# Kernel optimization log

Measured on AMD Instinct MI355X. Metric: run time of the kernel, lower is better.

Reference implementation:

```python
import jax, jax.numpy as jnp
from jax import lax
import numpy as np

B, T, H, FUT = 2048, 1024, 128, 64

def setup_inputs() -> dict:
    key = jax.random.key(0)
    ks = jax.random.split(key, 7)
    s = 1.0 / np.sqrt(H)
    return {
        "x": jax.random.normal(ks[0], (B, T), dtype=jnp.float32),
        "W_ih": jax.random.uniform(ks[1], (H, 1), jnp.float32, -s, s),
        "W_hh": jax.random.uniform(ks[2], (H, H), jnp.float32, -s, s),
        "b_ih": jax.random.uniform(ks[3], (H,), jnp.float32, -s, s),
        "b_hh": jax.random.uniform(ks[4], (H,), jnp.float32, -s, s),
        "W_out": jax.random.uniform(ks[5], (1, H), jnp.float32, -s, s),
        "b_out": jax.random.uniform(ks[6], (1,), jnp.float32, -s, s),
        "future": FUT,
    }

def reference(x, W_ih, W_hh, b_ih, b_hh, W_out, b_out, future):
    n_samples = x.shape[0]
    n_hidden = W_hh.shape[0]
    h0 = jnp.zeros((n_samples, n_hidden), dtype=x.dtype)
    bias = b_ih + b_hh  # [H]

    def cell(h, inp):  # inp: [B] scalar input per sample
        # RNNCell: h' = tanh(x @ W_ih^T + b_ih + h @ W_hh^T + b_hh)
        h_new = jnp.tanh(inp[:, None] * W_ih[:, 0][None, :] + h @ W_hh.T + bias)
        out = h_new @ W_out.T + b_out  # [B, 1]
        return h_new, out[:, 0]

    # Teacher-forced steps over the input sequence
    h_last, outs = lax.scan(cell, h0, x.T)  # outs: [T, B]

    def fstep(carry, _):
        h, o = carry
        h_new, o_new = cell(h, o)
        return (h_new, o_new), o_new

    (_, _), fouts = lax.scan(fstep, (h_last, outs[-1]), None, length=future)  # [future, B]

    return jnp.concatenate([outs, fouts], axis=0).T  # [B, T+future]
```

## Files before the change

### kernel.cpp

```cpp
#include <hip/hip_runtime.h>
#include <stdint.h>
#include <math.h>


#define TLEN  1024
#define FUT   64
#define HID   128
#define SPB   4
#define NT    256
#define NSTEP (TLEN + FUT)

typedef float f32x4 __attribute__((ext_vector_type(4)));
typedef _Float16 f16x8 __attribute__((ext_vector_type(8)));
typedef uint32_t u32x4 __attribute__((ext_vector_type(4)));

__device__ __forceinline__ f16x8 asf16(u32x4 v) {
    return __builtin_bit_cast(f16x8, v);
}
__device__ __forceinline__ float fast_tanh(float v) {
    return 1.0f - 2.0f / (__expf(2.0f * v) + 1.0f);
}

__global__ __launch_bounds__(NT, 2) void rnn_kernel(
    const float* __restrict__ x,
    const float* __restrict__ W_ih,
    const float* __restrict__ W_hh,
    const float* __restrict__ b_ih,
    const float* __restrict__ b_hh,
    const float* __restrict__ W_out,
    const float* __restrict__ b_out,
    float* __restrict__ out)
{
    __shared__ __align__(16) unsigned short hbuf[2][SPB * HID];
    __shared__ __align__(16) float xstg[128][8];
    __shared__ __align__(16) float ring[2][SPB][68];

    const int tid  = threadIdx.x;
    const int lane = tid & 63;
    const int wid  = tid >> 6;
    const int l15  = lane & 15;
    const int g    = lane >> 4;
    const int s0   = blockIdx.x * SPB;

    const int j0 = 32 * wid + l15;
    const int j1 = j0 + 16;
    f16x8 W0[4], W1[4], Wo[4];
    {
        const float* r0 = W_hh + (size_t)j0 * HID;
        const float* r1 = W_hh + (size_t)j1 * HID;
        #pragma unroll
        for (int kt = 0; kt < 4; ++kt) {
            #pragma unroll
            for (int e = 0; e < 8; ++e) {
                const int k = 16 * e + 4 * kt + g;
                W0[kt][e] = (_Float16)r0[k];
                W1[kt][e] = (_Float16)r1[k];
                Wo[kt][e] = (l15 == 0) ? (_Float16)W_out[k] : (_Float16)0.0f;
            }
        }
    }
    const float bias0 = b_ih[j0] + b_hh[j0];
    const float bias1 = b_ih[j1] + b_hh[j1];
    const float wih0  = W_ih[j0], wih1 = W_ih[j1];
    const float bo    = b_out[0];

    const int s_ = l15 >> 2;
    int aoff[4];
    #pragma unroll
    for (int kt = 0; kt < 4; ++kt)
        aoff[kt] = s_ * 256 + (((4 * kt + g) * 16) ^ (s_ << 5));
    const int woff = g * 256 + ((l15 * 16 + wid * 4) ^ (g << 5));

    for (int idx = tid; idx < SPB * HID; idx += NT)
        ((uint32_t*)hbuf)[idx] = 0;
    __syncthreads();

    u32x4 A_[4];
    #pragma unroll
    for (int kt = 0; kt < 4; ++kt) A_[kt] = (u32x4){0, 0, 0, 0};

    #pragma unroll 2
    for (int i = 0; i < TLEN; ++i) {
        const int p = i & 1;

        if ((i & 127) == 0) {
            #pragma unroll
            for (int pass = 0; pass < 2; ++pass) {
                const int idx = pass * NT + tid;
                const int t = idx & 127, s = idx >> 7;
                xstg[t][s] = x[(size_t)(s0 + s) * TLEN + (i + t)];
            }
            __syncthreads();
        }
        if (i > 64 && (i & 63) == 1 && tid < 16 * SPB) {
            const int q = ((i - 65) >> 6) & 1;
            const int s = tid >> 4, c4 = (tid & 15) * 4;
            const f32x4 v = *(const f32x4*)&ring[q][s][c4];
            *(f32x4*)&out[(size_t)(s0 + s) * NSTEP + (i - 65) + c4] = v;
        }

        const char* hb = (const char*)hbuf[p];
        if ((l15 & 3) == 0) {
            #pragma unroll
            for (int kt = 0; kt < 4; ++kt)
                A_[kt] = *(const u32x4*)(hb + aoff[kt]);
        }

        f32x4 sA = {0.f,0.f,0.f,0.f}, sB = sA;
        #pragma unroll
        for (int kt = 0; kt < 4; ++kt) {
            sA = __builtin_amdgcn_mfma_f32_16x16x32_f16(asf16(A_[kt]), W0[kt], sA, 0, 0, 0);
            sB = __builtin_amdgcn_mfma_f32_16x16x32_f16(asf16(A_[kt]), W1[kt], sB, 0, 0, 0);
        }
        if (wid == 0) {
            f32x4 ov = {0.f,0.f,0.f,0.f};
            #pragma unroll
            for (int kt = 0; kt < 4; ++kt)
                ov = __builtin_amdgcn_mfma_f32_16x16x32_f16(asf16(A_[kt]), Wo[kt], ov, 0, 0, 0);
            if (i > 0 && l15 == 0)
                ring[((i - 1) >> 6) & 1][g][(i - 1) & 63] = ov[0] + bo;
        }

        const float in = xstg[i & 127][g];
        const float h0 = fast_tanh(sA[0] + bias0 + in * wih0);
        const float h1 = fast_tanh(sB[0] + bias1 + in * wih1);
        const uint32_t pv = (uint32_t)__builtin_bit_cast(unsigned short, (_Float16)h0)
                          | ((uint32_t)__builtin_bit_cast(unsigned short, (_Float16)h1) << 16);
        *(uint32_t*)((char*)hbuf[p ^ 1] + woff) = pv;

        __syncthreads();
    }

    #pragma unroll 2
    for (int i = TLEN; i < NSTEP; ++i) {
        const int p = i & 1;

        if ((i & 63) == 1 && tid < 16 * SPB) {
            const int q = ((i - 65) >> 6) & 1;
            const int s = tid >> 4, c4 = (tid & 15) * 4;
            const f32x4 v = *(const f32x4*)&ring[q][s][c4];
            *(f32x4*)&out[(size_t)(s0 + s) * NSTEP + (i - 65) + c4] = v;
        }

        const char* hb = (const char*)hbuf[p];
        if ((l15 & 3) == 0) {
            #pragma unroll
            for (int kt = 0; kt < 4; ++kt)
                A_[kt] = *(const u32x4*)(hb + aoff[kt]);
        }

        f32x4 sA = {0.f,0.f,0.f,0.f}, sB = sA, ov = sA;
        #pragma unroll
        for (int kt = 0; kt < 4; ++kt) {
            sA = __builtin_amdgcn_mfma_f32_16x16x32_f16(asf16(A_[kt]), W0[kt], sA, 0, 0, 0);
            sB = __builtin_amdgcn_mfma_f32_16x16x32_f16(asf16(A_[kt]), W1[kt], sB, 0, 0, 0);
            ov = __builtin_amdgcn_mfma_f32_16x16x32_f16(asf16(A_[kt]), Wo[kt], ov, 0, 0, 0);
        }
        const float oval = ov[0] + bo;
        if (wid == 0 && l15 == 0)
            ring[((i - 1) >> 6) & 1][g][(i - 1) & 63] = oval;

        const float in = __shfl(oval, g << 4);
        const float h0 = fast_tanh(sA[0] + bias0 + in * wih0);
        const float h1 = fast_tanh(sB[0] + bias1 + in * wih1);
        const uint32_t pv = (uint32_t)__builtin_bit_cast(unsigned short, (_Float16)h0)
                          | ((uint32_t)__builtin_bit_cast(unsigned short, (_Float16)h1) << 16);
        *(uint32_t*)((char*)hbuf[p ^ 1] + woff) = pv;

        __syncthreads();
    }

    {
        const char* hb = (const char*)hbuf[NSTEP & 1];
        if ((l15 & 3) == 0) {
            #pragma unroll
            for (int kt = 0; kt < 4; ++kt)
                A_[kt] = *(const u32x4*)(hb + aoff[kt]);
        }
        f32x4 ov = {0.f,0.f,0.f,0.f};
        #pragma unroll
        for (int kt = 0; kt < 4; ++kt)
            ov = __builtin_amdgcn_mfma_f32_16x16x32_f16(asf16(A_[kt]), Wo[kt], ov, 0, 0, 0);
        if (wid == 0 && l15 == 0)
            ring[0][g][63] = ov[0] + bo;
    }
    __syncthreads();
    if (tid < 16 * SPB) {
        const int s = tid >> 4, c4 = (tid & 15) * 4;
        const f32x4 v = *(const f32x4*)&ring[0][s][c4];
        *(f32x4*)&out[(size_t)(s0 + s) * NSTEP + TLEN + c4] = v;
    }
}

extern "C" void kernel_launch(void* const* d_in, const int* in_sizes, int n_in,
                              void* d_out, int out_size, void* d_ws, size_t ws_size,
                              hipStream_t stream) {
    const float* x     = (const float*)d_in[0];
    const float* W_ih  = (const float*)d_in[1];
    const float* W_hh  = (const float*)d_in[2];
    const float* b_ih  = (const float*)d_in[3];
    const float* b_hh  = (const float*)d_in[4];
    const float* W_out = (const float*)d_in[5];
    const float* b_out = (const float*)d_in[6];
    float* out = (float*)d_out;

    dim3 grid(2048 / SPB);
    dim3 block(NT);
    rnn_kernel<<<grid, block, 0, stream>>>(x, W_ih, W_hh, b_ih, b_hh,
                                           W_out, b_out, out);
}
```

Baseline: 391.2 us.

## Split hidden units across 8 waves with one MFMA tile per wave

```diff
diff --git a/kernel.cpp b/kernel.cpp
--- a/kernel.cpp
+++ b/kernel.cpp
@@ -7,7 +7,7 @@
 #define FUT   64
 #define HID   128
 #define SPB   4
-#define NT    256
+#define NT    512
 #define NSTEP (TLEN + FUT)
 
 typedef float f32x4 __attribute__((ext_vector_type(4)));
@@ -21,7 +21,7 @@
     return 1.0f - 2.0f / (__expf(2.0f * v) + 1.0f);
 }
 
-__global__ __launch_bounds__(NT, 2) void rnn_kernel(
+__global__ __launch_bounds__(NT, 4) void rnn_kernel(
     const float* __restrict__ x,
     const float* __restrict__ W_ih,
     const float* __restrict__ W_hh,
@@ -42,26 +42,22 @@
     const int g    = lane >> 4;
     const int s0   = blockIdx.x * SPB;
 
-    const int j0 = 32 * wid + l15;
-    const int j1 = j0 + 16;
-    f16x8 W0[4], W1[4], Wo[4];
+    const int j = 16 * wid + l15;
+    f16x8 W0[4], Wo[4];
     {
-        const float* r0 = W_hh + (size_t)j0 * HID;
-        const float* r1 = W_hh + (size_t)j1 * HID;
+        const float* r0 = W_hh + (size_t)j * HID;
         #pragma unroll
         for (int kt = 0; kt < 4; ++kt) {
             #pragma unroll
             for (int e = 0; e < 8; ++e) {
                 const int k = 16 * e + 4 * kt + g;
                 W0[kt][e] = (_Float16)r0[k];
-                W1[kt][e] = (_Float16)r1[k];
                 Wo[kt][e] = (l15 == 0) ? (_Float16)W_out[k] : (_Float16)0.0f;
             }
         }
     }
-    const float bias0 = b_ih[j0] + b_hh[j0];
-    const float bias1 = b_ih[j1] + b_hh[j1];
-    const float wih0  = W_ih[j0], wih1 = W_ih[j1];
+    const float bias0 = b_ih[j] + b_hh[j];
+    const float wih0  = W_ih[j];
     const float bo    = b_out[0];
 
     const int s_ = l15 >> 2;
@@ -69,7 +65,7 @@
     #pragma unroll
     for (int kt = 0; kt < 4; ++kt)
         aoff[kt] = s_ * 256 + (((4 * kt + g) * 16) ^ (s_ << 5));
-    const int woff = g * 256 + ((l15 * 16 + wid * 4) ^ (g << 5));
+    const int woff = g * 256 + ((l15 * 16 + 2 * wid) ^ (g << 5));
 
     for (int idx = tid; idx < SPB * HID; idx += NT)
         ((uint32_t*)hbuf)[idx] = 0;
@@ -84,12 +80,8 @@
         const int p = i & 1;
 
         if ((i & 127) == 0) {
-            #pragma unroll
-            for (int pass = 0; pass < 2; ++pass) {
-                const int idx = pass * NT + tid;
-                const int t = idx & 127, s = idx >> 7;
-                xstg[t][s] = x[(size_t)(s0 + s) * TLEN + (i + t)];
-            }
+            const int t = tid & 127, s = tid >> 7;
+            xstg[t][s] = x[(size_t)(s0 + s) * TLEN + (i + t)];
             __syncthreads();
         }
         if (i > 64 && (i & 63) == 1 && tid < 16 * SPB) {
@@ -106,27 +98,20 @@
                 A_[kt] = *(const u32x4*)(hb + aoff[kt]);
         }
 
-        f32x4 sA = {0.f,0.f,0.f,0.f}, sB = sA;
+        f32x4 sA = {0.f,0.f,0.f,0.f}, ov = sA;
         #pragma unroll
         for (int kt = 0; kt < 4; ++kt) {
             sA = __builtin_amdgcn_mfma_f32_16x16x32_f16(asf16(A_[kt]), W0[kt], sA, 0, 0, 0);
-            sB = __builtin_amdgcn_mfma_f32_16x16x32_f16(asf16(A_[kt]), W1[kt], sB, 0, 0, 0);
+            ov = __builtin_amdgcn_mfma_f32_16x16x32_f16(asf16(A_[kt]), Wo[kt], ov, 0, 0, 0);
         }
-        if (wid == 0) {
-            f32x4 ov = {0.f,0.f,0.f,0.f};
-            #pragma unroll
-            for (int kt = 0; kt < 4; ++kt)
-                ov = __builtin_amdgcn_mfma_f32_16x16x32_f16(asf16(A_[kt]), Wo[kt], ov, 0, 0, 0);
-            if (i > 0 && l15 == 0)
-                ring[((i - 1) >> 6) & 1][g][(i - 1) & 63] = ov[0] + bo;
-        }
+
+        if (i > 0 && wid == 0 && l15 == 0)
+            ring[((i - 1) >> 6) & 1][g][(i - 1) & 63] = ov[0] + bo;
 
         const float in = xstg[i & 127][g];
         const float h0 = fast_tanh(sA[0] + bias0 + in * wih0);
-        const float h1 = fast_tanh(sB[0] + bias1 + in * wih1);
-        const uint32_t pv = (uint32_t)__builtin_bit_cast(unsigned short, (_Float16)h0)
-                          | ((uint32_t)__builtin_bit_cast(unsigned short, (_Float16)h1) << 16);
-        *(uint32_t*)((char*)hbuf[p ^ 1] + woff) = pv;
+        *(unsigned short*)((char*)hbuf[p ^ 1] + woff) =
+            __builtin_bit_cast(unsigned short, (_Float16)h0);
 
         __syncthreads();
     }
@@ -149,11 +134,10 @@
                 A_[kt] = *(const u32x4*)(hb + aoff[kt]);
         }
 
-        f32x4 sA = {0.f,0.f,0.f,0.f}, sB = sA, ov = sA;
+        f32x4 sA = {0.f,0.f,0.f,0.f}, ov = sA;
         #pragma unroll
         for (int kt = 0; kt < 4; ++kt) {
             sA = __builtin_amdgcn_mfma_f32_16x16x32_f16(asf16(A_[kt]), W0[kt], sA, 0, 0, 0);
-            sB = __builtin_amdgcn_mfma_f32_16x16x32_f16(asf16(A_[kt]), W1[kt], sB, 0, 0, 0);
             ov = __builtin_amdgcn_mfma_f32_16x16x32_f16(asf16(A_[kt]), Wo[kt], ov, 0, 0, 0);
         }
         const float oval = ov[0] + bo;
@@ -162,10 +146,8 @@
 
         const float in = __shfl(oval, g << 4);
         const float h0 = fast_tanh(sA[0] + bias0 + in * wih0);
-        const float h1 = fast_tanh(sB[0] + bias1 + in * wih1);
-        const uint32_t pv = (uint32_t)__builtin_bit_cast(unsigned short, (_Float16)h0)
-                          | ((uint32_t)__builtin_bit_cast(unsigned short, (_Float16)h1) << 16);
-        *(uint32_t*)((char*)hbuf[p ^ 1] + woff) = pv;
+        *(unsigned short*)((char*)hbuf[p ^ 1] + woff) =
+            __builtin_bit_cast(unsigned short, (_Float16)h0);
 
         __syncthreads();
     }
```

New measurement: 395.0 us. Within noise of the previous version (+1.0%).
